# Optimization experiments

Measured on AMD Instinct MI355X. Metric: run time of the kernel, lower is better.

Reference implementation:

```python
import jax, jax.numpy as jnp
import numpy as np

N_QUBITS = 4
N_LAYERS = 3
N_OUTPUTS = 4
BATCH = 1048576


def _ry(t):
    # RY(t) = [[cos(t/2), -sin(t/2)], [sin(t/2), cos(t/2)]]; t may be scalar or (B,)
    c = jnp.cos(t / 2)
    s = jnp.sin(t / 2)
    m = jnp.stack([jnp.stack([c, -s], -1), jnp.stack([s, c], -1)], -2)
    return m.astype(jnp.complex64)


def _rx(t):
    c = jnp.cos(t / 2).astype(jnp.complex64)
    s = jnp.sin(t / 2).astype(jnp.complex64)
    return jnp.stack([jnp.stack([c, -1j * s], -1), jnp.stack([-1j * s, c], -1)], -2)


def _rz(t):
    e = jnp.exp(-1j * t.astype(jnp.complex64) / 2)  # exp(-i t/2)
    z = jnp.zeros_like(e)
    return jnp.stack([jnp.stack([e, z], -1), jnp.stack([z, jnp.conj(e)], -1)], -2)


def _apply_1q(state, U, q):
    # shared 2x2 gate U on wire q; state: (B, 2,2,2,2)
    s = jnp.moveaxis(state, q + 1, -1)
    s = jnp.einsum('ij,...j->...i', U, s)
    return jnp.moveaxis(s, -1, q + 1)


def _apply_1q_batched(state, U, q):
    # per-sample 2x2 gate U: (B,2,2) on wire q
    s = jnp.moveaxis(state, q + 1, -1)  # (B, ..., 2)
    s = jnp.einsum('bij,b...j->b...i', U, s)
    return jnp.moveaxis(s, -1, q + 1)


def _apply_cnot(state, c, t):
    s = jnp.moveaxis(state, (c + 1, t + 1), (-2, -1))  # (..., ctrl, tgt)
    s = jnp.stack([s[..., 0, :], s[..., 1, ::-1]], axis=-2)
    return jnp.moveaxis(s, (-2, -1), (c + 1, t + 1))


def setup_inputs() -> dict:
    key = jax.random.key(0)
    kx, kw = jax.random.split(key)
    x = jax.random.normal(kx, (BATCH, 2), dtype=jnp.float32)
    weights = jax.random.normal(kw, (N_LAYERS, N_QUBITS, 3), dtype=jnp.float32) * 0.1
    return {"x": x, "weights": weights}


def reference(x, weights):
    B = x.shape[0]
    # |0...0> state, batched
    state = jnp.zeros((B,) + (2,) * N_QUBITS, jnp.complex64)
    state = state.at[(slice(None),) + (0,) * N_QUBITS].set(1.0)
    # data encoding: RY(inputs[i % 2]) on wire i (per-sample angles)
    for i in range(N_QUBITS):
        state = _apply_1q_batched(state, _ry(x[:, i % 2]), i)
    # variational layers (shared angles)
    for l in range(N_LAYERS):
        for i in range(N_QUBITS):
            state = _apply_1q(state, _rx(weights[l, i, 0]), i)
            state = _apply_1q(state, _ry(weights[l, i, 1]), i)
            state = _apply_1q(state, _rz(weights[l, i, 2]), i)
        for i in range(N_QUBITS):
            state = _apply_cnot(state, i, (i + 1) % N_QUBITS)
    probs = state.real ** 2 + state.imag ** 2  # (B,2,2,2,2)
    outs = []
    for q in range(N_OUTPUTS):
        p = jnp.moveaxis(probs, q + 1, 1).reshape(B, 2, -1).sum(-1)
        outs.append(p[:, 0] - p[:, 1])  # <Z_q>
    return jnp.stack(outs, -1)  # (B, N_OUTPUTS)
```

## Files before the change

kernel.cpp:

```cpp
#include <hip/hip_runtime.h>
#include <hip/hip_bf16.h>


__device__ __forceinline__ float2 mul2(float2 a, float2 b) {
    return make_float2(a.x * b.x, a.y * b.y);
}
__device__ __forceinline__ float2 fma2(float s, float2 a, float2 b) {
    return make_float2(fmaf(s, a.x, b.x), fmaf(s, a.y, b.y));
}

__global__ __launch_bounds__(1024) void qnn_fused(const float4* __restrict__ x4,
                                                  const float* __restrict__ w,
                                                  float4* __restrict__ out,
                                                  int B) {
    __shared__ float Ur[16][16];
    __shared__ float Ui[16][16];
    __shared__ __align__(16) float Csh[100];
    const int t = threadIdx.x;

    if (t < 100) Csh[t] = 0.0f;

    if (t < 16) {
        float ar[16], ai[16];
#pragma unroll
        for (int i = 0; i < 16; i++) { ar[i] = (i == t) ? 1.0f : 0.0f; ai[i] = 0.0f; }

#pragma unroll
        for (int l = 0; l < 3; l++) {
#pragma unroll
            for (int wq = 0; wq < 4; wq++) {
                const int st = 1 << (3 - wq);
                float th, s, c;
                th = w[(l * 4 + wq) * 3 + 0] * 0.5f;
                __sincosf(th, &s, &c);
#pragma unroll
                for (int lo = 0; lo < 16; lo++) if (!(lo & st)) {
                    const int hi = lo | st;
                    const float arl = ar[lo], ail = ai[lo], arh = ar[hi], aih = ai[hi];
                    ar[lo] = c * arl + s * aih;
                    ai[lo] = c * ail - s * arh;
                    ar[hi] = c * arh + s * ail;
                    ai[hi] = c * aih - s * arl;
                }
                th = w[(l * 4 + wq) * 3 + 1] * 0.5f;
                __sincosf(th, &s, &c);
#pragma unroll
                for (int lo = 0; lo < 16; lo++) if (!(lo & st)) {
                    const int hi = lo | st;
                    const float arl = ar[lo], ail = ai[lo], arh = ar[hi], aih = ai[hi];
                    ar[lo] = c * arl - s * arh;
                    ai[lo] = c * ail - s * aih;
                    ar[hi] = s * arl + c * arh;
                    ai[hi] = s * ail + c * aih;
                }
                th = w[(l * 4 + wq) * 3 + 2] * 0.5f;
                __sincosf(th, &s, &c);
#pragma unroll
                for (int lo = 0; lo < 16; lo++) if (!(lo & st)) {
                    const int hi = lo | st;
                    const float arl = ar[lo], ail = ai[lo], arh = ar[hi], aih = ai[hi];
                    ar[lo] = c * arl + s * ail;
                    ai[lo] = c * ail - s * arl;
                    ar[hi] = c * arh - s * aih;
                    ai[hi] = c * aih + s * arh;
                }
            }
#pragma unroll
            for (int ci = 0; ci < 4; ci++) {
                const int cst = 1 << (3 - ci);
                const int tst = 1 << (3 - ((ci + 1) & 3));
#pragma unroll
                for (int k = 0; k < 16; k++) if ((k & cst) && !(k & tst)) {
                    const int k2 = k | tst;
                    const float tr = ar[k], ti = ai[k];
                    ar[k] = ar[k2]; ai[k] = ai[k2];
                    ar[k2] = tr;    ai[k2] = ti;
                }
            }
        }
#pragma unroll
        for (int i = 0; i < 16; i++) { Ur[i][t] = ar[i]; Ui[i][t] = ai[i]; }
    }
    __syncthreads();

    if (t < 256) {
        const int i = t >> 4;
        const int j = t & 15;
        float m0 = 0.f, m1 = 0.f, m2 = 0.f, m3 = 0.f;
#pragma unroll
        for (int k = 0; k < 16; k++) {
            const float r = Ur[k][i] * Ur[k][j] + Ui[k][i] * Ui[k][j];
            m0 += ((k >> 3) & 1) ? -r : r;
            m1 += ((k >> 2) & 1) ? -r : r;
            m2 += ((k >> 1) & 1) ? -r : r;
            m3 += ((k >> 0) & 1) ? -r : r;
        }
        const int mm = ((i >> 3) & 1) + ((i >> 1) & 1) + ((j >> 3) & 1) + ((j >> 1) & 1);
        const int nn = ((i >> 2) & 1) + (i & 1) + ((j >> 2) & 1) + (j & 1);
        const int mn4 = (mm * 5 + nn) * 4;
        atomicAdd(&Csh[mn4 + 0], m0);
        atomicAdd(&Csh[mn4 + 1], m1);
        atomicAdd(&Csh[mn4 + 2], m2);
        atomicAdd(&Csh[mn4 + 3], m3);
    }
    __syncthreads();

    const float4* __restrict__ Csh4 = (const float4*)Csh;

    const int bs = blockIdx.x * 4096;

    if (bs + 4096 <= B) {
#pragma unroll
        for (int k = 0; k < 2; k++) {
            const float4 f4 = x4[(bs >> 1) + k * 1024 + t];
            float2 s0, c0, s1, c1;
            __sincosf(f4.x * 0.5f, &s0.x, &c0.x);
            __sincosf(f4.z * 0.5f, &s0.y, &c0.y);
            __sincosf(f4.y * 0.5f, &s1.x, &c1.x);
            __sincosf(f4.w * 0.5f, &s1.y, &c1.y);

            const float2 cc0 = mul2(c0, c0), ss0 = mul2(s0, s0), cs0 = mul2(c0, s0);
            const float2 cc1 = mul2(c1, c1), ss1 = mul2(s1, s1), cs1 = mul2(c1, s1);
            const float2 p0[5] = { mul2(cc0, cc0), mul2(cc0, cs0), mul2(cs0, cs0),
                                   mul2(cs0, ss0), mul2(ss0, ss0) };
            const float2 p1[5] = { mul2(cc1, cc1), mul2(cc1, cs1), mul2(cs1, cs1),
                                   mul2(cs1, ss1), mul2(ss1, ss1) };

            float2 a0 = make_float2(0.f, 0.f), a1 = a0, a2 = a0, a3 = a0;
#pragma unroll
            for (int m = 0; m < 5; m++)
#pragma unroll
                for (int n = 0; n < 5; n++) {
                    const float4 cv = Csh4[m * 5 + n];
                    const float2 pp = mul2(p0[m], p1[n]);
                    a0 = fma2(cv.x, pp, a0);
                    a1 = fma2(cv.y, pp, a1);
                    a2 = fma2(cv.z, pp, a2);
                    a3 = fma2(cv.w, pp, a3);
                }
            const int s = bs + 2 * (k * 1024 + t);
            out[s]     = make_float4(a0.x, a1.x, a2.x, a3.x);
            out[s + 1] = make_float4(a0.y, a1.y, a2.y, a3.y);
        }
    } else {
        const float2* __restrict__ x2 = (const float2*)x4;
#pragma unroll
        for (int k = 0; k < 4; k++) {
            const int s = bs + k * 1024 + t;
            if (s < B) {
                const float2 xv = x2[s];
                float st0, ct0, st1, ct1;
                __sincosf(xv.x * 0.5f, &st0, &ct0);
                __sincosf(xv.y * 0.5f, &st1, &ct1);
                const float cc0 = ct0 * ct0, ss0 = st0 * st0, cs0 = ct0 * st0;
                const float cc1 = ct1 * ct1, ss1 = st1 * st1, cs1 = ct1 * st1;
                const float q0[5] = { cc0 * cc0, cc0 * cs0, cs0 * cs0, cs0 * ss0, ss0 * ss0 };
                const float q1[5] = { cc1 * cc1, cc1 * cs1, cs1 * cs1, cs1 * ss1, ss1 * ss1 };
                float o0 = 0.f, o1 = 0.f, o2 = 0.f, o3 = 0.f;
#pragma unroll
                for (int m = 0; m < 5; m++)
#pragma unroll
                    for (int n = 0; n < 5; n++) {
                        const float4 cv = Csh4[m * 5 + n];
                        const float pp = q0[m] * q1[n];
                        o0 = fmaf(cv.x, pp, o0);
                        o1 = fmaf(cv.y, pp, o1);
                        o2 = fmaf(cv.z, pp, o2);
                        o3 = fmaf(cv.w, pp, o3);
                    }
                out[s] = make_float4(o0, o1, o2, o3);
            }
        }
    }
}

extern "C" void kernel_launch(void* const* d_in, const int* in_sizes, int n_in,
                              void* d_out, int out_size, void* d_ws, size_t ws_size,
                              hipStream_t stream) {
    const float* x = (const float*)d_in[0];
    const float* w = (const float*)d_in[1];
    const int B = in_sizes[0] / 2;

    int grid = (B + 4095) / 4096;
    if (grid < 1) grid = 1;
    qnn_fused<<<grid, 1024, 0, stream>>>((const float4*)x, w, (float4*)d_out, B);
}
```

Baseline: 84.19 us.

## Split coefficient setup into separate kernel and load coefficients into registers

The per-block 16x16 unitary construction and coefficient reduction move into a single-block setup kernel that writes 100 coefficients to workspace. The batch kernel then loads those coefficients into registers through scalar loads, with no shared memory or barriers. Blocks shrink to 256 threads with 1024 samples each, and memory access becomes contiguous float2 loads with coalesced float4 stores. This removes the redundant unitary computation every block used to do, at the price of an extra kernel launch and a serial dependency between the two kernels.

```diff
diff --git a/kernel.cpp b/kernel.cpp
--- a/kernel.cpp
+++ b/kernel.cpp
@@ -2,20 +2,11 @@
 #include <hip/hip_bf16.h>
 
 
-__device__ __forceinline__ float2 mul2(float2 a, float2 b) {
-    return make_float2(a.x * b.x, a.y * b.y);
-}
-__device__ __forceinline__ float2 fma2(float s, float2 a, float2 b) {
-    return make_float2(fmaf(s, a.x, b.x), fmaf(s, a.y, b.y));
-}
-
-__global__ __launch_bounds__(1024) void qnn_fused(const float4* __restrict__ x4,
-                                                  const float* __restrict__ w,
-                                                  float4* __restrict__ out,
-                                                  int B) {
+__global__ __launch_bounds__(256) void qnn_setup(const float* __restrict__ w,
+                                                 float* __restrict__ C_out) {
     __shared__ float Ur[16][16];
     __shared__ float Ui[16][16];
-    __shared__ __align__(16) float Csh[100];
+    __shared__ float Csh[100];
     const int t = threadIdx.x;
 
     if (t < 100) Csh[t] = 0.0f;
@@ -83,7 +74,7 @@
     }
     __syncthreads();
 
-    if (t < 256) {
+    {
         const int i = t >> 4;
         const int j = t & 15;
         float m0 = 0.f, m1 = 0.f, m2 = 0.f, m3 = 0.f;
@@ -104,20 +95,41 @@
         atomicAdd(&Csh[mn4 + 3], m3);
     }
     __syncthreads();
-
-    const float4* __restrict__ Csh4 = (const float4*)Csh;
-
-    const int bs = blockIdx.x * 4096;
-
-    if (bs + 4096 <= B) {
+    if (t < 100) C_out[t] = Csh[t];
+}
+
+
+__device__ __forceinline__ float2 mul2(float2 a, float2 b) {
+    return make_float2(a.x * b.x, a.y * b.y);
+}
+__device__ __forceinline__ float2 fma2(float s, float2 a, float2 b) {
+    return make_float2(fmaf(s, a.x, b.x), fmaf(s, a.y, b.y));
+}
+
+__global__ __launch_bounds__(256) void qnn_batch(const float2* __restrict__ x2,
+                                                 const float4* __restrict__ C4,
+                                                 float4* __restrict__ out,
+                                                 int B) {
+    float4 cv[25];
+#pragma unroll
+    for (int i = 0; i < 25; i++) cv[i] = C4[i];
+    __builtin_amdgcn_sched_barrier(0);
+
+    const int t = threadIdx.x;
+    const int bs = blockIdx.x * 1024;
+
+    if (bs + 1024 <= B) {
 #pragma unroll
         for (int k = 0; k < 2; k++) {
-            const float4 f4 = x4[(bs >> 1) + k * 1024 + t];
+            const int sA = bs + k * 512 + t;
+            const int sB = sA + 256;
+            const float2 xA = x2[sA];
+            const float2 xB = x2[sB];
             float2 s0, c0, s1, c1;
-            __sincosf(f4.x * 0.5f, &s0.x, &c0.x);
-            __sincosf(f4.z * 0.5f, &s0.y, &c0.y);
-            __sincosf(f4.y * 0.5f, &s1.x, &c1.x);
-            __sincosf(f4.w * 0.5f, &s1.y, &c1.y);
+            __sincosf(xA.x * 0.5f, &s0.x, &c0.x);
+            __sincosf(xB.x * 0.5f, &s0.y, &c0.y);
+            __sincosf(xA.y * 0.5f, &s1.x, &c1.x);
+            __sincosf(xB.y * 0.5f, &s1.y, &c1.y);
 
             const float2 cc0 = mul2(c0, c0), ss0 = mul2(s0, s0), cs0 = mul2(c0, s0);
             const float2 cc1 = mul2(c1, c1), ss1 = mul2(s1, s1), cs1 = mul2(c1, s1);
@@ -131,22 +143,20 @@
             for (int m = 0; m < 5; m++)
 #pragma unroll
                 for (int n = 0; n < 5; n++) {
-                    const float4 cv = Csh4[m * 5 + n];
+                    const float4 cvv = cv[m * 5 + n];
                     const float2 pp = mul2(p0[m], p1[n]);
-                    a0 = fma2(cv.x, pp, a0);
-                    a1 = fma2(cv.y, pp, a1);
-                    a2 = fma2(cv.z, pp, a2);
-                    a3 = fma2(cv.w, pp, a3);
-                }
-            const int s = bs + 2 * (k * 1024 + t);
-            out[s]     = make_float4(a0.x, a1.x, a2.x, a3.x);
-            out[s + 1] = make_float4(a0.y, a1.y, a2.y, a3.y);
+                    a0 = fma2(cvv.x, pp, a0);
+                    a1 = fma2(cvv.y, pp, a1);
+                    a2 = fma2(cvv.z, pp, a2);
+                    a3 = fma2(cvv.w, pp, a3);
+                }
+            out[sA] = make_float4(a0.x, a1.x, a2.x, a3.x);
+            out[sB] = make_float4(a0.y, a1.y, a2.y, a3.y);
         }
     } else {
-        const float2* __restrict__ x2 = (const float2*)x4;
 #pragma unroll
         for (int k = 0; k < 4; k++) {
-            const int s = bs + k * 1024 + t;
+            const int s = bs + k * 256 + t;
             if (s < B) {
                 const float2 xv = x2[s];
                 float st0, ct0, st1, ct1;
@@ -161,12 +171,12 @@
                 for (int m = 0; m < 5; m++)
 #pragma unroll
                     for (int n = 0; n < 5; n++) {
-                        const float4 cv = Csh4[m * 5 + n];
+                        const float4 cvv = cv[m * 5 + n];
                         const float pp = q0[m] * q1[n];
-                        o0 = fmaf(cv.x, pp, o0);
-                        o1 = fmaf(cv.y, pp, o1);
-                        o2 = fmaf(cv.z, pp, o2);
-                        o3 = fmaf(cv.w, pp, o3);
+                        o0 = fmaf(cvv.x, pp, o0);
+                        o1 = fmaf(cvv.y, pp, o1);
+                        o2 = fmaf(cvv.z, pp, o2);
+                        o3 = fmaf(cvv.w, pp, o3);
                     }
                 out[s] = make_float4(o0, o1, o2, o3);
             }
@@ -179,9 +189,13 @@
                               hipStream_t stream) {
     const float* x = (const float*)d_in[0];
     const float* w = (const float*)d_in[1];
+    float* C = (float*)d_ws;
     const int B = in_sizes[0] / 2;
 
-    int grid = (B + 4095) / 4096;
+    qnn_setup<<<1, 256, 0, stream>>>(w, C);
+
+    int grid = (B + 1023) / 1024;
     if (grid < 1) grid = 1;
-    qnn_fused<<<grid, 1024, 0, stream>>>((const float4*)x, w, (float4*)d_out, B);
-}
+    qnn_batch<<<grid, 256, 0, stream>>>((const float2*)x, (const float4*)C,
+                                        (float4*)d_out, B);
+}
```

Result: faster. 74.09 us (-12.0%).
